# Kernel tuning notes

Hardware: AMD Instinct MI355X
Metric: run time of the kernel (lower is better)

## Reference

```python
import jax, jax.numpy as jnp
import numpy as np

N = 100000
E = 1600000
D_IN = 50
D_H = 128
D_OUT = 128
EPS = 1e-5


def setup_inputs() -> dict:
    key = jax.random.key(0)
    ks = jax.random.split(key, 24)
    def w(k, shape, fan_in):
        return jax.random.normal(k, shape, jnp.float32) / np.sqrt(fan_in)
    inp = {
        'x': jax.random.normal(ks[0], (N, D_IN), jnp.float32),
        'edge_src': jax.random.randint(ks[1], (E,), 0, N, jnp.int32),
        'edge_dst': jax.random.randint(ks[2], (E,), 0, N, jnp.int32),
        # SAGEConv 1: D_IN -> D_H
        'Wl1': w(ks[3], (D_IN, D_H), D_IN), 'Wr1': w(ks[4], (D_IN, D_H), D_IN), 'b1': jnp.zeros((D_H,), jnp.float32),
        # SAGEConv 2: D_H -> D_H
        'Wl2': w(ks[5], (D_H, D_H), D_H), 'Wr2': w(ks[6], (D_H, D_H), D_H), 'b2': jnp.zeros((D_H,), jnp.float32),
        # SAGEConv 3: D_H -> D_OUT
        'Wl3': w(ks[7], (D_H, D_OUT), D_H), 'Wr3': w(ks[8], (D_H, D_OUT), D_H), 'b3': jnp.zeros((D_OUT,), jnp.float32),
        # skip linears (no bias)
        'Ws1': w(ks[9], (D_IN, D_H), D_IN), 'Ws2': w(ks[10], (D_IN, D_H), D_IN),
        # LayerNorm affine
        'lnw1': jnp.ones((D_H,), jnp.float32), 'lnb1': jnp.zeros((D_H,), jnp.float32),
        'lnw2': jnp.ones((D_H,), jnp.float32), 'lnb2': jnp.zeros((D_H,), jnp.float32),
        'lnw3': jnp.ones((D_OUT,), jnp.float32), 'lnb3': jnp.zeros((D_OUT,), jnp.float32),
        # PReLU scalar slopes (PyG init 0.25)
        'a1': jnp.float32(0.25), 'a2': jnp.float32(0.25), 'a3': jnp.float32(0.25),
    }
    return inp


def _sage(x, src, dst, Wl, Wr, b):
    # mean aggregation of source features at destinations, then linear + root
    msg = x[src]                                              # [E, d]
    agg = jax.ops.segment_sum(msg, dst, num_segments=N)       # [N, d]
    cnt = jax.ops.segment_sum(jnp.ones((src.shape[0],), x.dtype), dst, num_segments=N)
    mean = agg / jnp.maximum(cnt, 1.0)[:, None]
    return mean @ Wl + x @ Wr + b


def _graph_ln(x, w, b):
    # PyG LayerNorm mode='graph', batch=None: normalize over all nodes+channels
    xc = x - jnp.mean(x)
    std = jnp.sqrt(jnp.mean(xc * xc))
    return (xc / (std + EPS)) * w + b


def _prelu(x, a):
    return jnp.where(x >= 0, x, a * x)


def reference(x, edge_src, edge_dst, Wl1, Wr1, b1, Wl2, Wr2, b2, Wl3, Wr3, b3,
              Ws1, Ws2, lnw1, lnb1, lnw2, lnb2, lnw3, lnb3, a1, a2, a3):
    h1 = _sage(x, edge_src, edge_dst, Wl1, Wr1, b1)
    h1 = _prelu(_graph_ln(h1, lnw1, lnb1), a1)
    h2 = _sage(h1 + x @ Ws1, edge_src, edge_dst, Wl2, Wr2, b2)
    h2 = _prelu(_graph_ln(h2, lnw2, lnb2), a2)
    ret = _sage(h1 + h2 + x @ Ws2, edge_src, edge_dst, Wl3, Wr3, b3)
    ret = _prelu(_graph_ln(ret, lnw3, lnb3), a3)
    return ret
```

## Files before the change

kernel.cpp:

```cpp
#include <hip/hip_runtime.h>

#define D_IN 50
#define LN_EPS 1e-5f
#define BSH 8
#define MAXB 512

typedef __bf16 bf16_t;
typedef bf16_t bf16x8 __attribute__((ext_vector_type(8)));
typedef float f32x4_t __attribute__((ext_vector_type(4)));
typedef float f32x2_t __attribute__((ext_vector_type(2)));

#define STRIDE_ST 136

#define ACCP(r, A)                                                            \
    {                                                                         \
        A[0] += (f32x2_t){__uint_as_float((r).x << 16),                       \
                          __uint_as_float((r).x & 0xffff0000u)};              \
        A[1] += (f32x2_t){__uint_as_float((r).y << 16),                       \
                          __uint_as_float((r).y & 0xffff0000u)};              \
        A[2] += (f32x2_t){__uint_as_float((r).z << 16),                       \
                          __uint_as_float((r).z & 0xffff0000u)};              \
        A[3] += (f32x2_t){__uint_as_float((r).w << 16),                       \
                          __uint_as_float((r).w & 0xffff0000u)};              \
    }

__global__ void bucket_hist_k(const int* __restrict__ dst, int* __restrict__ bcnt,
                              double* __restrict__ lnacc, int e, int nb) {
    __shared__ int lh[MAXB];
    int t = threadIdx.x;
    if (blockIdx.x == 0 && t < 6) lnacc[t] = 0.0;
    for (int i = t; i < nb; i += 256) lh[i] = 0;
    __syncthreads();
    for (int i = blockIdx.x * 256 + t; i < e; i += gridDim.x * 256)
        atomicAdd(&lh[dst[i] >> BSH], 1);
    __syncthreads();
    for (int i = t; i < nb; i += 256) {
        int c = lh[i];
        if (c) atomicAdd(&bcnt[i * 16], c);
    }
}

__global__ void bscan_k(const int* __restrict__ bcnt, int* __restrict__ boff,
                        int* __restrict__ bpos, int nb, int e) {
    __shared__ int l[MAXB];
    int t = threadIdx.x;
    l[t] = (t < nb) ? bcnt[t * 16] : 0;
    __syncthreads();
    for (int off = 1; off < MAXB; off <<= 1) {
        int v = (t >= off) ? l[t - off] : 0;
        __syncthreads();
        l[t] += v;
        __syncthreads();
    }
    int excl = (t > 0) ? l[t - 1] : 0;
    if (t < nb) { boff[t] = excl; bpos[t * 16] = excl; }
    if (t == 0) boff[nb] = e;
}

__global__ void scatter_k(const int* __restrict__ src, const int* __restrict__ dst,
                          int* __restrict__ bpos, unsigned* __restrict__ pool,
                          int e, int nb) {
    __shared__ int lh[MAXB];
    __shared__ int lcur[MAXB];
    int t = threadIdx.x;
    for (int i = t; i < nb; i += 256) lh[i] = 0;
    __syncthreads();
    int chunk = (e + gridDim.x - 1) / gridDim.x;
    int s = blockIdx.x * chunk;
    int en = min(e, s + chunk);
    for (int i = s + t; i < en; i += 256)
        atomicAdd(&lh[dst[i] >> BSH], 1);
    __syncthreads();
    for (int i = t; i < nb; i += 256) {
        int c = lh[i];
        lcur[i] = c ? atomicAdd(&bpos[i * 16], c) : 0;
    }
    __syncthreads();
    for (int i = s + t; i < en; i += 256) {
        int d = dst[i];
        int p = atomicAdd(&lcur[d >> BSH], 1);
        pool[p] = (unsigned)src[i] | ((unsigned)(d & 255) << 17);
    }
}

__global__ void nhist_cfill_k(const unsigned* __restrict__ pool, const int* __restrict__ boff,
                              int* __restrict__ rp, int* __restrict__ col, int n) {
    __shared__ int lc[256];
    __shared__ int ls[256];
    __shared__ int lpos[256];
    int b = blockIdx.x, t = threadIdx.x;
    lc[t] = 0;
    __syncthreads();
    int s = boff[b], e = boff[b + 1];
    for (int i = s + t; i < e; i += 256) atomicAdd(&lc[pool[i] >> 17], 1);
    __syncthreads();
    int v = lc[t];
    ls[t] = v;
    __syncthreads();
    for (int off = 1; off < 256; off <<= 1) {
        int x = (t >= off) ? ls[t - off] : 0;
        __syncthreads();
        ls[t] += x;
        __syncthreads();
    }
    int excl = ls[t] - v;
    int nd = (b << BSH) + t;
    if (nd < n) rp[nd] = s + excl;
    if (nd == n - 1) rp[n] = e;
    lpos[t] = s + excl;
    __syncthreads();
    for (int i = s + t; i < e; i += 256) {
        unsigned pk = pool[i];
        int slot = atomicAdd(&lpos[pk >> 17], 1);
        col[slot] = (int)(pk & 0x1FFFFu);
    }
}

struct ConvDesc { const float* w; bf16_t* o; int kin; int kpad; };
struct ConvArgs { ConvDesc d[8]; };

__global__ void conv_w_k(ConvArgs args) {
    ConvDesc d = args.d[blockIdx.y];
    int i = blockIdx.x * 256 + threadIdx.x;
    int tot = 128 * d.kpad;
    if (i >= tot) return;
    int n = i / d.kpad, k = i - n * d.kpad;
    float v = (k < d.kin) ? d.w[(size_t)k * 128 + n] : 0.f;
    d.o[i] = (bf16_t)v;
}

__global__ void conv_x_k(const float* __restrict__ x, bf16_t* __restrict__ xb, int n) {
    int i = blockIdx.x * 256 + threadIdx.x;
    if (i >= n * 64) return;
    int node = i >> 6, k = i & 63;
    xb[i] = (k < D_IN) ? (bf16_t)x[node * D_IN + k] : (bf16_t)0.f;
}

__global__ void agg_bf64_k(const bf16_t* __restrict__ feat, const int* __restrict__ rp,
                           const int* __restrict__ col, bf16_t* __restrict__ mean, int n) {
    int wid = (blockIdx.x * blockDim.x + threadIdx.x) >> 6;
    int lane = threadIdx.x & 63;
    if (wid >= n) return;
    int start = rp[wid], end = rp[wid + 1];
    int lc = lane & 7;
    int g = lane >> 3;
    f32x2_t accA[4], accB[4];
#pragma unroll
    for (int k = 0; k < 4; k++) { accA[k] = (f32x2_t){0.f, 0.f}; accB[k] = (f32x2_t){0.f, 0.f}; }
    int e = start + g;
    if (e + 8 < end) {
        int i0 = col[e], i1 = col[e + 8];
        for (; e + 24 < end; e += 16) {
            uint4 r0 = *(const uint4*)(feat + (size_t)i0 * 64 + lc * 8);
            uint4 r1 = *(const uint4*)(feat + (size_t)i1 * 64 + lc * 8);
            i0 = col[e + 16];
            i1 = col[e + 24];
            ACCP(r0, accA);
            ACCP(r1, accB);
        }
        uint4 r0 = *(const uint4*)(feat + (size_t)i0 * 64 + lc * 8);
        uint4 r1 = *(const uint4*)(feat + (size_t)i1 * 64 + lc * 8);
        ACCP(r0, accA);
        ACCP(r1, accB);
        e += 16;
    }
    for (; e < end; e += 8) {
        uint4 r0 = *(const uint4*)(feat + (size_t)col[e] * 64 + lc * 8);
        ACCP(r0, accA);
    }
#pragma unroll
    for (int k = 0; k < 4; k++) accA[k] += accB[k];
    float aL[4], aH[4];
#pragma unroll
    for (int k = 0; k < 4; k++) { aL[k] = accA[k].x; aH[k] = accA[k].y; }
#pragma unroll
    for (int off = 8; off < 64; off <<= 1) {
#pragma unroll
        for (int k = 0; k < 4; k++) {
            aL[k] += __shfl_xor(aL[k], off);
            aH[k] += __shfl_xor(aH[k], off);
        }
    }
    int c = end - start;
    float invc = 1.f / (float)(c > 0 ? c : 1);
    if (lane < 8) {
        bf16x8 o;
#pragma unroll
        for (int k = 0; k < 4; k++) {
            o[2 * k] = (bf16_t)(aL[k] * invc);
            o[2 * k + 1] = (bf16_t)(aH[k] * invc);
        }
        *(bf16x8*)(mean + (size_t)wid * 64 + lc * 8) = o;
    }
}

__global__ void agg_bf128_k(const bf16_t* __restrict__ feat, const int* __restrict__ rp,
                            const int* __restrict__ col, bf16_t* __restrict__ mean, int n) {
    int wid = (blockIdx.x * blockDim.x + threadIdx.x) >> 6;
    int lane = threadIdx.x & 63;
    if (wid >= n) return;
    int start = rp[wid], end = rp[wid + 1];
    int lc = lane & 15;
    int g = lane >> 4;
    f32x2_t accA[4], accB[4];
#pragma unroll
    for (int k = 0; k < 4; k++) { accA[k] = (f32x2_t){0.f, 0.f}; accB[k] = (f32x2_t){0.f, 0.f}; }
    int e = start + g;
    if (e + 4 < end) {
        int i0 = col[e], i1 = col[e + 4];
        for (; e + 12 < end; e += 8) {
            uint4 r0 = *(const uint4*)(feat + (size_t)i0 * 128 + lc * 8);
            uint4 r1 = *(const uint4*)(feat + (size_t)i1 * 128 + lc * 8);
            i0 = col[e + 8];
            i1 = col[e + 12];
            ACCP(r0, accA);
            ACCP(r1, accB);
        }
        uint4 r0 = *(const uint4*)(feat + (size_t)i0 * 128 + lc * 8);
        uint4 r1 = *(const uint4*)(feat + (size_t)i1 * 128 + lc * 8);
        ACCP(r0, accA);
        ACCP(r1, accB);
        e += 8;
    }
    for (; e < end; e += 4) {
        uint4 r0 = *(const uint4*)(feat + (size_t)col[e] * 128 + lc * 8);
        ACCP(r0, accA);
    }
#pragma unroll
    for (int k = 0; k < 4; k++) accA[k] += accB[k];
    float aL[4], aH[4];
#pragma unroll
    for (int k = 0; k < 4; k++) { aL[k] = accA[k].x; aH[k] = accA[k].y; }
#pragma unroll
    for (int off = 16; off < 64; off <<= 1) {
#pragma unroll
        for (int k = 0; k < 4; k++) {
            aL[k] += __shfl_xor(aL[k], off);
            aH[k] += __shfl_xor(aH[k], off);
        }
    }
    int c = end - start;
    float invc = 1.f / (float)(c > 0 ? c : 1);
    if (lane < 16) {
        bf16x8 o;
#pragma unroll
        for (int k = 0; k < 4; k++) {
            o[2 * k] = (bf16_t)(aL[k] * invc);
            o[2 * k + 1] = (bf16_t)(aH[k] * invc);
        }
        *(bf16x8*)(mean + (size_t)wid * 128 + lc * 8) = o;
    }
}

template <int KPAD, bool DUAL>
__global__ __launch_bounds__(256) void mfma_gemm_k(
    const bf16_t* __restrict__ A, const bf16_t* __restrict__ B,
    const bf16_t* __restrict__ WlT, const bf16_t* __restrict__ WrT,
    const float* __restrict__ bias,
    bf16_t* __restrict__ out, double* __restrict__ lnacc, int M) {
    constexpr int KC = KPAD / 32;
    constexpr int WELE = 8 * KC * 64 * 8;
    __shared__ bf16_t lwl[WELE];
    __shared__ __align__(16) bf16_t lst[4][16 * STRIDE_ST];
    __shared__ float rsum[4], rsum2[4];

    const int tid = threadIdx.x;
    for (int ch = tid; ch < 8 * KC * 64; ch += 256) {
        int nt = ch / (KC * 64);
        int rem = ch - nt * (KC * 64);
        int c = rem >> 6;
        int ln = rem & 63;
        int mm = ln & 15, qq = ln >> 4;
        size_t srcoff = (size_t)(nt * 16 + mm) * KPAD + c * 32 + qq * 8;
        *(bf16x8*)&lwl[ch * 8] = *(const bf16x8*)(WlT + srcoff);
    }
    __syncthreads();

    const int w = tid >> 6;
    const int wid = blockIdx.x * 4 + w;
    const int lane = tid & 63;
    const int row0 = wid * 32;
    const int m = lane & 15;
    const int q = lane >> 4;
    const bool act = row0 < M;

    float lsum = 0.f, lsum2 = 0.f;
    if (act) {
        bf16x8 af[2][KC], bfr[DUAL ? 2 : 1][DUAL ? KC : 1];
#pragma unroll
        for (int s = 0; s < 2; s++) {
            const bf16_t* ar = A + (size_t)(row0 + s * 16 + m) * KPAD + q * 8;
#pragma unroll
            for (int c = 0; c < KC; c++) af[s][c] = *(const bf16x8*)(ar + c * 32);
            if (DUAL) {
                const bf16_t* br = B + (size_t)(row0 + s * 16 + m) * KPAD + q * 8;
#pragma unroll
                for (int c = 0; c < KC; c++) bfr[s][c] = *(const bf16x8*)(br + c * 32);
            }
        }
        bf16_t* st = lst[w];
#pragma unroll
        for (int s = 0; s < 2; s++) {
#pragma unroll
            for (int nt = 0; nt < 8; nt++) {
                f32x4_t acc = {0.f, 0.f, 0.f, 0.f};
#pragma unroll
                for (int c = 0; c < KC; c++) {
                    bf16x8 wl = *(const bf16x8*)&lwl[((nt * KC + c) * 64 + lane) * 8];
                    acc = __builtin_amdgcn_mfma_f32_16x16x32_bf16(af[s][c], wl, acc, 0, 0, 0);
                }
                if (DUAL) {
#pragma unroll
                    for (int c = 0; c < KC; c++) {
                        size_t woff = (size_t)(nt * 16 + m) * KPAD + c * 32 + q * 8;
                        bf16x8 wr = *(const bf16x8*)(WrT + woff);
                        acc = __builtin_amdgcn_mfma_f32_16x16x32_bf16(bfr[s][c], wr, acc, 0, 0, 0);
                    }
                }
                float bv = bias ? bias[nt * 16 + m] : 0.f;
#pragma unroll
                for (int r = 0; r < 4; r++) {
                    float o = acc[r] + bv;
                    int row = row0 + s * 16 + q * 4 + r;
                    if (row < M) { lsum += o; lsum2 += o * o; }
                    st[(q * 4 + r) * STRIDE_ST + nt * 16 + m] = (bf16_t)o;
                }
            }
            int rowbase = row0 + s * 16;
#pragma unroll
            for (int k = 0; k < 4; k++) {
                int chunk = k * 64 + lane;
                int rr = chunk >> 4;
                int co = (chunk & 15) * 8;
                int row = rowbase + rr;
                bf16x8 v = *(bf16x8*)&st[rr * STRIDE_ST + co];
                if (row < M) *(bf16x8*)(out + (size_t)row * 128 + co) = v;
            }
        }
    }
    for (int off = 32; off > 0; off >>= 1) {
        lsum += __shfl_down(lsum, off);
        lsum2 += __shfl_down(lsum2, off);
    }
    if (lane == 0) { rsum[w] = lsum; rsum2[w] = lsum2; }
    __syncthreads();
    if (tid == 0) {
        double s = (double)rsum[0] + (double)rsum[1] + (double)rsum[2] + (double)rsum[3];
        double s2 = (double)rsum2[0] + (double)rsum2[1] + (double)rsum2[2] + (double)rsum2[3];
        unsafeAtomicAdd(&lnacc[0], s);
        unsafeAtomicAdd(&lnacc[1], s2);
    }
}

__global__ __launch_bounds__(256) void mfma_gemm3_k(
    const bf16_t* __restrict__ A, const bf16_t* __restrict__ B,
    const bf16_t* __restrict__ WlT, const bf16_t* __restrict__ WrT,
    const bf16_t* __restrict__ Ws1T, const bf16_t* __restrict__ Ws2T,
    const float* __restrict__ bias,
    bf16_t* __restrict__ outP, bf16_t* __restrict__ outC1, bf16_t* __restrict__ outC2,
    double* __restrict__ lnacc, int M) {
    constexpr int KC = 2;
    constexpr int WELE = 8 * KC * 64 * 8;
    __shared__ bf16_t lwl[WELE];
    __shared__ bf16_t lwr[WELE];
    __shared__ __align__(16) bf16_t lst[4][16 * STRIDE_ST];
    __shared__ float rsum[4], rsum2[4];

    const int tid = threadIdx.x;
    for (int ch = tid; ch < 8 * KC * 64; ch += 256) {
        int nt = ch / (KC * 64);
        int rem = ch - nt * (KC * 64);
        int c = rem >> 6;
        int ln = rem & 63;
        int mm = ln & 15, qq = ln >> 4;
        size_t srcoff = (size_t)(nt * 16 + mm) * 64 + c * 32 + qq * 8;
        *(bf16x8*)&lwl[ch * 8] = *(const bf16x8*)(WlT + srcoff);
        *(bf16x8*)&lwr[ch * 8] = *(const bf16x8*)(WrT + srcoff);
    }
    __syncthreads();

    const int w = tid >> 6;
    const int wid = blockIdx.x * 4 + w;
    const int lane = tid & 63;
    const int row0 = wid * 32;
    const int m = lane & 15;
    const int q = lane >> 4;
    const bool act = row0 < M;

    float lsum = 0.f, lsum2 = 0.f;
    if (act) {
        bf16x8 af[2][KC], bfr[2][KC];
#pragma unroll
        for (int s = 0; s < 2; s++) {
            const bf16_t* ar = A + (size_t)(row0 + s * 16 + m) * 64 + q * 8;
            const bf16_t* br = B + (size_t)(row0 + s * 16 + m) * 64 + q * 8;
#pragma unroll
            for (int c = 0; c < KC; c++) {
                af[s][c] = *(const bf16x8*)(ar + c * 32);
                bfr[s][c] = *(const bf16x8*)(br + c * 32);
            }
        }
        bf16_t* st = lst[w];

#pragma unroll
        for (int s = 0; s < 2; s++) {
#pragma unroll
            for (int nt = 0; nt < 8; nt++) {
                f32x4_t acc = {0.f, 0.f, 0.f, 0.f};
#pragma unroll
                for (int c = 0; c < KC; c++) {
                    int wi = ((nt * KC + c) * 64 + lane) * 8;
                    bf16x8 wl = *(const bf16x8*)&lwl[wi];
                    bf16x8 wr = *(const bf16x8*)&lwr[wi];
                    acc = __builtin_amdgcn_mfma_f32_16x16x32_bf16(af[s][c], wl, acc, 0, 0, 0);
                    acc = __builtin_amdgcn_mfma_f32_16x16x32_bf16(bfr[s][c], wr, acc, 0, 0, 0);
                }
                float bv = bias[nt * 16 + m];
#pragma unroll
                for (int r = 0; r < 4; r++) {
                    float o = acc[r] + bv;
                    int row = row0 + s * 16 + q * 4 + r;
                    if (row < M) { lsum += o; lsum2 += o * o; }
                    st[(q * 4 + r) * STRIDE_ST + nt * 16 + m] = (bf16_t)o;
                }
            }
            int rowbase = row0 + s * 16;
#pragma unroll
            for (int k = 0; k < 4; k++) {
                int chunk = k * 64 + lane;
                int rr = chunk >> 4;
                int co = (chunk & 15) * 8;
                int row = rowbase + rr;
                bf16x8 v = *(bf16x8*)&st[rr * STRIDE_ST + co];
                if (row < M) *(bf16x8*)(outP + (size_t)row * 128 + co) = v;
            }
        }

#pragma unroll
        for (int p = 0; p < 2; p++) {
            const bf16_t* WT = (p == 0) ? Ws1T : Ws2T;
            bf16_t* outC = (p == 0) ? outC1 : outC2;
#pragma unroll
            for (int s = 0; s < 2; s++) {
#pragma unroll
                for (int nt = 0; nt < 8; nt++) {
                    f32x4_t acc = {0.f, 0.f, 0.f, 0.f};
#pragma unroll
                    for (int c = 0; c < KC; c++) {
                        size_t woff = (size_t)(nt * 16 + m) * 64 + c * 32 + q * 8;
                        bf16x8 wv = *(const bf16x8*)(WT + woff);
                        acc = __builtin_amdgcn_mfma_f32_16x16x32_bf16(bfr[s][c], wv, acc, 0, 0, 0);
                    }
#pragma unroll
                    for (int r = 0; r < 4; r++)
                        st[(q * 4 + r) * STRIDE_ST + nt * 16 + m] = (bf16_t)acc[r];
                }
                int rowbase = row0 + s * 16;
#pragma unroll
                for (int k = 0; k < 4; k++) {
                    int chunk = k * 64 + lane;
                    int rr = chunk >> 4;
                    int co = (chunk & 15) * 8;
                    int row = rowbase + rr;
                    bf16x8 v = *(bf16x8*)&st[rr * STRIDE_ST + co];
                    if (row < M) *(bf16x8*)(outC + (size_t)row * 128 + co) = v;
                }
            }
        }
    }
    for (int off = 32; off > 0; off >>= 1) {
        lsum += __shfl_down(lsum, off);
        lsum2 += __shfl_down(lsum2, off);
    }
    if (lane == 0) { rsum[w] = lsum; rsum2[w] = lsum2; }
    __syncthreads();
    if (tid == 0) {
        double s = (double)rsum[0] + (double)rsum[1] + (double)rsum[2] + (double)rsum[3];
        double s2 = (double)rsum2[0] + (double)rsum2[1] + (double)rsum2[2] + (double)rsum2[3];
        unsafeAtomicAdd(&lnacc[0], s);
        unsafeAtomicAdd(&lnacc[1], s2);
    }
}

template <int MODE>
__global__ void ln_prelu_k(const bf16_t* __restrict__ pre, const bf16_t* __restrict__ h1in,
                           const bf16_t* __restrict__ s,
                           const float* __restrict__ lnw, const float* __restrict__ lnb,
                           const float* __restrict__ a_ptr, const double* __restrict__ acc,
                           void* __restrict__ out0v, void* __restrict__ out1v, int total) {
    int i = blockIdx.x * blockDim.x + threadIdx.x;
    if (i * 8 >= total) return;
    double cinv = 1.0 / (double)total;
    double mm = acc[0] * cinv;
    double var = acc[1] * cinv - mm * mm;
    float stdv = (float)sqrt(var > 0.0 ? var : 0.0);
    float scale = 1.0f / (stdv + LN_EPS);
    float mf = (float)mm;
    float a = a_ptr[0];
    int c8 = i & 15;
    float4 w0 = ((const float4*)lnw)[c8 * 2];
    float4 w1 = ((const float4*)lnw)[c8 * 2 + 1];
    float4 b0 = ((const float4*)lnb)[c8 * 2];
    float4 b1 = ((const float4*)lnb)[c8 * 2 + 1];
    float wv[8] = {w0.x, w0.y, w0.z, w0.w, w1.x, w1.y, w1.z, w1.w};
    float bv[8] = {b0.x, b0.y, b0.z, b0.w, b1.x, b1.y, b1.z, b1.w};
    bf16x8 p8 = ((const bf16x8*)pre)[i];
    float h[8];
#pragma unroll
    for (int k = 0; k < 8; k++) {
        float v = ((float)p8[k] - mf) * scale * wv[k] + bv[k];
        h[k] = v >= 0.f ? v : a * v;
    }
    if (MODE == 1) {
        bf16x8 hb, tb;
        bf16x8 sv = ((const bf16x8*)s)[i];
#pragma unroll
        for (int k = 0; k < 8; k++) {
            hb[k] = (bf16_t)h[k];
            tb[k] = (bf16_t)(h[k] + (float)sv[k]);
        }
        ((bf16x8*)out0v)[i] = hb;
        ((bf16x8*)out1v)[i] = tb;
    } else if (MODE == 2) {
        bf16x8 hv = ((const bf16x8*)h1in)[i];
        bf16x8 sv = ((const bf16x8*)s)[i];
        bf16x8 tb;
#pragma unroll
        for (int k = 0; k < 8; k++)
            tb[k] = (bf16_t)((float)hv[k] + h[k] + (float)sv[k]);
        ((bf16x8*)out0v)[i] = tb;
    } else {
        float4 o0 = {h[0], h[1], h[2], h[3]};
        float4 o1 = {h[4], h[5], h[6], h[7]};
        ((float4*)out0v)[i * 2] = o0;
        ((float4*)out0v)[i * 2 + 1] = o1;
    }
}

extern "C" void kernel_launch(void* const* d_in, const int* in_sizes, int n_in,
                              void* d_out, int out_size, void* d_ws, size_t ws_size,
                              hipStream_t stream) {
    const float* x    = (const float*)d_in[0];
    const int*   esrc = (const int*)d_in[1];
    const int*   edst = (const int*)d_in[2];
    const float* Wl1  = (const float*)d_in[3];
    const float* Wr1  = (const float*)d_in[4];
    const float* b1   = (const float*)d_in[5];
    const float* Wl2  = (const float*)d_in[6];
    const float* Wr2  = (const float*)d_in[7];
    const float* b2   = (const float*)d_in[8];
    const float* Wl3  = (const float*)d_in[9];
    const float* Wr3  = (const float*)d_in[10];
    const float* b3   = (const float*)d_in[11];
    const float* Ws1  = (const float*)d_in[12];
    const float* Ws2  = (const float*)d_in[13];
    const float* lnw1 = (const float*)d_in[14];
    const float* lnb1 = (const float*)d_in[15];
    const float* lnw2 = (const float*)d_in[16];
    const float* lnb2 = (const float*)d_in[17];
    const float* lnw3 = (const float*)d_in[18];
    const float* lnb3 = (const float*)d_in[19];
    const float* a1   = (const float*)d_in[20];
    const float* a2   = (const float*)d_in[21];
    const float* a3   = (const float*)d_in[22];

    const int N = in_sizes[0] / D_IN;
    const int E = in_sizes[1];
    const int NB = (N + 255) >> BSH;

    char* ws = (char*)d_ws;
    size_t off = 0;
    auto alloc = [&](size_t bytes) -> void* {
        void* p = ws + off;
        off += (bytes + 255) & ~(size_t)255;
        return p;
    };
    bf16_t* xb   = (bf16_t*)alloc((size_t)N * 64 * 2);
    bf16_t* mean = (bf16_t*)alloc((size_t)N * 128 * 2);
    bf16_t* PRE  = (bf16_t*)alloc((size_t)N * 128 * 2);
    bf16_t* C1   = (bf16_t*)alloc((size_t)N * 128 * 2);
    bf16_t* C2   = (bf16_t*)alloc((size_t)N * 128 * 2);
    bf16_t* h1b  = (bf16_t*)alloc((size_t)N * 128 * 2);
    bf16_t* TB   = (bf16_t*)alloc((size_t)N * 128 * 2);
    bf16_t* WT   = (bf16_t*)alloc((size_t)(4 * 128 * 64 + 4 * 128 * 128) * 2);
    int* rp   = (int*)alloc((size_t)(N + 1) * 4);
    int* col  = (int*)alloc((size_t)E * 4);
    int* bcnt = (int*)alloc((size_t)MAXB * 16 * 4);
    int* boff = (int*)alloc((size_t)(MAXB + 1) * 4);
    int* bpos = (int*)alloc((size_t)MAXB * 16 * 4);
    unsigned* pool = (unsigned*)alloc((size_t)E * 4);
    double* lnacc = (double*)alloc(6 * 8);

    bf16_t* Wl1T = WT;
    bf16_t* Wr1T = Wl1T + 128 * 64;
    bf16_t* Ws1T = Wr1T + 128 * 64;
    bf16_t* Ws2T = Ws1T + 128 * 64;
    bf16_t* Wl2T = Ws2T + 128 * 64;
    bf16_t* Wr2T = Wl2T + 128 * 128;
    bf16_t* Wl3T = Wr2T + 128 * 128;
    bf16_t* Wr3T = Wl3T + 128 * 128;

    hipMemsetAsync(bcnt, 0, (size_t)MAXB * 16 * 4, stream);

    bucket_hist_k<<<256, 256, 0, stream>>>(edst, bcnt, lnacc, E, NB);
    bscan_k<<<1, MAXB, 0, stream>>>(bcnt, boff, bpos, NB, E);
    scatter_k<<<256, 256, 0, stream>>>(esrc, edst, bpos, pool, E, NB);
    nhist_cfill_k<<<NB, 256, 0, stream>>>(pool, boff, rp, col, N);

    ConvArgs ca;
    ca.d[0] = {Wl1, Wl1T, 50, 64};
    ca.d[1] = {Wr1, Wr1T, 50, 64};
    ca.d[2] = {Ws1, Ws1T, 50, 64};
    ca.d[3] = {Ws2, Ws2T, 50, 64};
    ca.d[4] = {Wl2, Wl2T, 128, 128};
    ca.d[5] = {Wr2, Wr2T, 128, 128};
    ca.d[6] = {Wl3, Wl3T, 128, 128};
    ca.d[7] = {Wr3, Wr3T, 128, 128};
    conv_w_k<<<dim3(64, 8), 256, 0, stream>>>(ca);
    conv_x_k<<<(N * 64 + 255) / 256, 256, 0, stream>>>(x, xb, N);

    const int aggBlocks = ((N * 64) + 255) / 256;
    const int tiles = (N + 31) / 32;
    const int gemmBlocks = (tiles + 3) / 4;
    const int lnBlocks = (N * 128 / 8 + 255) / 256;
    const int total = N * 128;

    agg_bf64_k<<<aggBlocks, 256, 0, stream>>>(xb, rp, col, mean, N);
    mfma_gemm3_k<<<gemmBlocks, 256, 0, stream>>>(
        mean, xb, Wl1T, Wr1T, Ws1T, Ws2T, b1, PRE, C1, C2, lnacc + 0, N);
    ln_prelu_k<1><<<lnBlocks, 256, 0, stream>>>(
        PRE, nullptr, C1, lnw1, lnb1, a1, lnacc + 0, h1b, TB, total);

    agg_bf128_k<<<aggBlocks, 256, 0, stream>>>(TB, rp, col, mean, N);
    mfma_gemm_k<128, true><<<gemmBlocks, 256, 0, stream>>>(
        mean, TB, Wl2T, Wr2T, b2, PRE, lnacc + 2, N);
    ln_prelu_k<2><<<lnBlocks, 256, 0, stream>>>(
        PRE, h1b, C2, lnw2, lnb2, a2, lnacc + 2, TB, nullptr, total);

    agg_bf128_k<<<aggBlocks, 256, 0, stream>>>(TB, rp, col, mean, N);
    mfma_gemm_k<128, true><<<gemmBlocks, 256, 0, stream>>>(
        mean, TB, Wl3T, Wr3T, b3, PRE, lnacc + 4, N);
    ln_prelu_k<3><<<lnBlocks, 256, 0, stream>>>(
        PRE, nullptr, nullptr, lnw3, lnb3, a3, lnacc + 4, d_out, nullptr, total);
}
```

Baseline: 547.2 us.

## Spread LN atomics over slots, stage Wr in LDS, unroll gather, direct stores

Sums for graph LayerNorm statistics now go into 64 padded slots per layer instead of one double pair, and each LN block reduces the slots itself. This is meant to cut atomic contention on a single address. The GEMM now stages Wr in LDS alongside Wl and shares each weight fragment across both 16-row subtiles. It also drops the LDS output staging and writes bf16 scalars straight to global memory, which can make stores less coalesced. The 128-wide aggregation loop is unrolled to four independent gathers per iteration.

```diff
diff --git a/kernel.cpp b/kernel.cpp
--- a/kernel.cpp
+++ b/kernel.cpp
@@ -4,6 +4,7 @@
 #define LN_EPS 1e-5f
 #define BSH 8
 #define MAXB 512
+#define NSLOT 64
 
 typedef __bf16 bf16_t;
 typedef bf16_t bf16x8 __attribute__((ext_vector_type(8)));
@@ -28,7 +29,10 @@
                               double* __restrict__ lnacc, int e, int nb) {
     __shared__ int lh[MAXB];
     int t = threadIdx.x;
-    if (blockIdx.x == 0 && t < 6) lnacc[t] = 0.0;
+    if (blockIdx.x == 0 && t < 3 * NSLOT) {
+        lnacc[t * 8] = 0.0;
+        lnacc[t * 8 + 1] = 0.0;
+    }
     for (int i = t; i < nb; i += 256) lh[i] = 0;
     __syncthreads();
     for (int i = blockIdx.x * 256 + t; i < e; i += gridDim.x * 256)
@@ -202,29 +206,35 @@
     int start = rp[wid], end = rp[wid + 1];
     int lc = lane & 15;
     int g = lane >> 4;
+    const uint* fp = (const uint*)feat + lc * 4;
     f32x2_t accA[4], accB[4];
 #pragma unroll
     for (int k = 0; k < 4; k++) { accA[k] = (f32x2_t){0.f, 0.f}; accB[k] = (f32x2_t){0.f, 0.f}; }
     int e = start + g;
-    if (e + 4 < end) {
-        int i0 = col[e], i1 = col[e + 4];
-        for (; e + 12 < end; e += 8) {
-            uint4 r0 = *(const uint4*)(feat + (size_t)i0 * 128 + lc * 8);
-            uint4 r1 = *(const uint4*)(feat + (size_t)i1 * 128 + lc * 8);
-            i0 = col[e + 8];
-            i1 = col[e + 12];
-            ACCP(r0, accA);
-            ACCP(r1, accB);
-        }
-        uint4 r0 = *(const uint4*)(feat + (size_t)i0 * 128 + lc * 8);
-        uint4 r1 = *(const uint4*)(feat + (size_t)i1 * 128 + lc * 8);
+    int ng = (e < end) ? (((end - 1 - e) >> 2) + 1) : 0;
+    int it = 0;
+    for (; it + 4 <= ng; it += 4, e += 16) {
+        int a = col[e], b = col[e + 4], c = col[e + 8], d = col[e + 12];
+        uint4 r0 = *(const uint4*)(fp + (size_t)a * 64);
+        uint4 r1 = *(const uint4*)(fp + (size_t)b * 64);
+        uint4 r2 = *(const uint4*)(fp + (size_t)c * 64);
+        uint4 r3 = *(const uint4*)(fp + (size_t)d * 64);
         ACCP(r0, accA);
         ACCP(r1, accB);
-        e += 8;
-    }
-    for (; e < end; e += 4) {
-        uint4 r0 = *(const uint4*)(feat + (size_t)col[e] * 128 + lc * 8);
+        ACCP(r2, accA);
+        ACCP(r3, accB);
+    }
+    int rem = ng - it;
+    if (rem > 0) {
+        int a = col[e];
+        int b = (rem > 1) ? col[e + 4] : a;
+        int c = (rem > 2) ? col[e + 8] : b;
+        uint4 r0 = *(const uint4*)(fp + (size_t)a * 64);
+        uint4 r1 = *(const uint4*)(fp + (size_t)b * 64);
+        uint4 r2 = *(const uint4*)(fp + (size_t)c * 64);
         ACCP(r0, accA);
+        if (rem > 1) ACCP(r1, accB);
+        if (rem > 2) ACCP(r2, accA);
     }
 #pragma unroll
     for (int k = 0; k < 4; k++) accA[k] += accB[k];
@@ -261,7 +271,7 @@
     constexpr int KC = KPAD / 32;
     constexpr int WELE = 8 * KC * 64 * 8;
     __shared__ bf16_t lwl[WELE];
-    __shared__ __align__(16) bf16_t lst[4][16 * STRIDE_ST];
+    __shared__ bf16_t lwr[DUAL ? WELE : 8];
     __shared__ float rsum[4], rsum2[4];
 
     const int tid = threadIdx.x;
@@ -273,6 +283,7 @@
         int mm = ln & 15, qq = ln >> 4;
         size_t srcoff = (size_t)(nt * 16 + mm) * KPAD + c * 32 + qq * 8;
         *(bf16x8*)&lwl[ch * 8] = *(const bf16x8*)(WlT + srcoff);
+        if (DUAL) *(bf16x8*)&lwr[ch * 8] = *(const bf16x8*)(WrT + srcoff);
     }
     __syncthreads();
 
@@ -298,43 +309,37 @@
                 for (int c = 0; c < KC; c++) bfr[s][c] = *(const bf16x8*)(br + c * 32);
             }
         }
-        bf16_t* st = lst[w];
-#pragma unroll
-        for (int s = 0; s < 2; s++) {
-#pragma unroll
-            for (int nt = 0; nt < 8; nt++) {
-                f32x4_t acc = {0.f, 0.f, 0.f, 0.f};
+#pragma unroll
+        for (int nt = 0; nt < 8; nt++) {
+            f32x4_t acc0 = {0.f, 0.f, 0.f, 0.f};
+            f32x4_t acc1 = {0.f, 0.f, 0.f, 0.f};
+#pragma unroll
+            for (int c = 0; c < KC; c++) {
+                bf16x8 wv = *(const bf16x8*)&lwl[((nt * KC + c) * 64 + lane) * 8];
+                acc0 = __builtin_amdgcn_mfma_f32_16x16x32_bf16(af[0][c], wv, acc0, 0, 0, 0);
+                acc1 = __builtin_amdgcn_mfma_f32_16x16x32_bf16(af[1][c], wv, acc1, 0, 0, 0);
+            }
+            if (DUAL) {
 #pragma unroll
                 for (int c = 0; c < KC; c++) {
-                    bf16x8 wl = *(const bf16x8*)&lwl[((nt * KC + c) * 64 + lane) * 8];
-                    acc = __builtin_amdgcn_mfma_f32_16x16x32_bf16(af[s][c], wl, acc, 0, 0, 0);
+                    bf16x8 wv = *(const bf16x8*)&lwr[((nt * KC + c) * 64 + lane) * 8];
+                    acc0 = __builtin_amdgcn_mfma_f32_16x16x32_bf16(bfr[0][c], wv, acc0, 0, 0, 0);
+                    acc1 = __builtin_amdgcn_mfma_f32_16x16x32_bf16(bfr[1][c], wv, acc1, 0, 0, 0);
                 }
-                if (DUAL) {
-#pragma unroll
-                    for (int c = 0; c < KC; c++) {
-                        size_t woff = (size_t)(nt * 16 + m) * KPAD + c * 32 + q * 8;
-                        bf16x8 wr = *(const bf16x8*)(WrT + woff);
-                        acc = __builtin_amdgcn_mfma_f32_16x16x32_bf16(bfr[s][c], wr, acc, 0, 0, 0);
+            }
+            float bv = bias ? bias[nt * 16 + m] : 0.f;
+#pragma unroll
+            for (int s = 0; s < 2; s++) {
+                f32x4_t* ap = (s == 0) ? &acc0 : &acc1;
+#pragma unroll
+                for (int r = 0; r < 4; r++) {
+                    int row = row0 + s * 16 + q * 4 + r;
+                    if (row < M) {
+                        float o = (*ap)[r] + bv;
+                        out[(size_t)row * 128 + nt * 16 + m] = (bf16_t)o;
+                        lsum += o; lsum2 += o * o;
                     }
                 }
-                float bv = bias ? bias[nt * 16 + m] : 0.f;
-#pragma unroll
-                for (int r = 0; r < 4; r++) {
-                    float o = acc[r] + bv;
-                    int row = row0 + s * 16 + q * 4 + r;
-                    if (row < M) { lsum += o; lsum2 += o * o; }
-                    st[(q * 4 + r) * STRIDE_ST + nt * 16 + m] = (bf16_t)o;
-                }
-            }
-            int rowbase = row0 + s * 16;
-#pragma unroll
-            for (int k = 0; k < 4; k++) {
-                int chunk = k * 64 + lane;
-                int rr = chunk >> 4;
-                int co = (chunk & 15) * 8;
-                int row = rowbase + rr;
-                bf16x8 v = *(bf16x8*)&st[rr * STRIDE_ST + co];
-                if (row < M) *(bf16x8*)(out + (size_t)row * 128 + co) = v;
             }
         }
     }
@@ -347,8 +352,9 @@
     if (tid == 0) {
         double s = (double)rsum[0] + (double)rsum[1] + (double)rsum[2] + (double)rsum[3];
         double s2 = (double)rsum2[0] + (double)rsum2[1] + (double)rsum2[2] + (double)rsum2[3];
-        unsafeAtomicAdd(&lnacc[0], s);
-        unsafeAtomicAdd(&lnacc[1], s2);
+        int slot = (blockIdx.x & (NSLOT - 1)) * 8;
+        unsafeAtomicAdd(&lnacc[slot], s);
+        unsafeAtomicAdd(&lnacc[slot + 1], s2);
     }
 }
 
@@ -477,8 +483,9 @@
     if (tid == 0) {
         double s = (double)rsum[0] + (double)rsum[1] + (double)rsum[2] + (double)rsum[3];
         double s2 = (double)rsum2[0] + (double)rsum2[1] + (double)rsum2[2] + (double)rsum2[3];
-        unsafeAtomicAdd(&lnacc[0], s);
-        unsafeAtomicAdd(&lnacc[1], s2);
+        int slot = (blockIdx.x & (NSLOT - 1)) * 8;
+        unsafeAtomicAdd(&lnacc[slot], s);
+        unsafeAtomicAdd(&lnacc[slot + 1], s2);
     }
 }
 
@@ -488,11 +495,23 @@
                            const float* __restrict__ lnw, const float* __restrict__ lnb,
                            const float* __restrict__ a_ptr, const double* __restrict__ acc,
                            void* __restrict__ out0v, void* __restrict__ out1v, int total) {
-    int i = blockIdx.x * blockDim.x + threadIdx.x;
+    __shared__ double ssum, ssum2;
+    int t = threadIdx.x;
+    if (t < 64) {
+        double a = acc[t * 8];
+        double b = acc[t * 8 + 1];
+        for (int off = 32; off > 0; off >>= 1) {
+            a += __shfl_down(a, off);
+            b += __shfl_down(b, off);
+        }
+        if (t == 0) { ssum = a; ssum2 = b; }
+    }
+    __syncthreads();
+    int i = blockIdx.x * blockDim.x + t;
     if (i * 8 >= total) return;
     double cinv = 1.0 / (double)total;
-    double mm = acc[0] * cinv;
-    double var = acc[1] * cinv - mm * mm;
+    double mm = ssum * cinv;
+    double var = ssum2 * cinv - mm * mm;
     float stdv = (float)sqrt(var > 0.0 ? var : 0.0);
     float scale = 1.0f / (stdv + LN_EPS);
     float mf = (float)mm;
@@ -589,7 +608,7 @@
     int* boff = (int*)alloc((size_t)(MAXB + 1) * 4);
     int* bpos = (int*)alloc((size_t)MAXB * 16 * 4);
     unsigned* pool = (unsigned*)alloc((size_t)E * 4);
-    double* lnacc = (double*)alloc(6 * 8);
+    double* lnacc = (double*)alloc((size_t)3 * NSLOT * 8 * 8);
 
     bf16_t* Wl1T = WT;
     bf16_t* Wr1T = Wl1T + 128 * 64;
@@ -624,22 +643,25 @@
     const int gemmBlocks = (tiles + 3) / 4;
     const int lnBlocks = (N * 128 / 8 + 255) / 256;
     const int total = N * 128;
+    double* acc1 = lnacc;
+    double* acc2 = lnacc + NSLOT * 8;
+    double* acc3 = lnacc + 2 * NSLOT * 8;
 
     agg_bf64_k<<<aggBlocks, 256, 0, stream>>>(xb, rp, col, mean, N);
     mfma_gemm3_k<<<gemmBlocks, 256, 0, stream>>>(
-        mean, xb, Wl1T, Wr1T, Ws1T, Ws2T, b1, PRE, C1, C2, lnacc + 0, N);
+        mean, xb, Wl1T, Wr1T, Ws1T, Ws2T, b1, PRE, C1, C2, acc1, N);
     ln_prelu_k<1><<<lnBlocks, 256, 0, stream>>>(
-        PRE, nullptr, C1, lnw1, lnb1, a1, lnacc + 0, h1b, TB, total);
+        PRE, nullptr, C1, lnw1, lnb1, a1, acc1, h1b, TB, total);
 
     agg_bf128_k<<<aggBlocks, 256, 0, stream>>>(TB, rp, col, mean, N);
     mfma_gemm_k<128, true><<<gemmBlocks, 256, 0, stream>>>(
-        mean, TB, Wl2T, Wr2T, b2, PRE, lnacc + 2, N);
+        mean, TB, Wl2T, Wr2T, b2, PRE, acc2, N);
     ln_prelu_k<2><<<lnBlocks, 256, 0, stream>>>(
-        PRE, h1b, C2, lnw2, lnb2, a2, lnacc + 2, TB, nullptr, total);
+        PRE, h1b, C2, lnw2, lnb2, a2, acc2, TB, nullptr, total);
 
     agg_bf128_k<<<aggBlocks, 256, 0, stream>>>(TB, rp, col, mean, N);
     mfma_gemm_k<128, true><<<gemmBlocks, 256, 0, stream>>>(
-        mean, TB, Wl3T, Wr3T, b3, PRE, lnacc + 4, N);
+        mean, TB, Wl3T, Wr3T, b3, PRE, acc3, N);
     ln_prelu_k<3><<<lnBlocks, 256, 0, stream>>>(
-        PRE, nullptr, nullptr, lnw3, lnb3, a3, lnacc + 4, d_out, nullptr, total);
-}
+        PRE, nullptr, nullptr, lnw3, lnb3, a3, acc3, d_out, nullptr, total);
+}
```

Result: faster. 521.1 us (median of 2 runs) (-4.8%).
